# Kernel tuning notes

Hardware: AMD Instinct MI355X
Metric: run time of the kernel (lower is better)

## Reference

```python
import jax, jax.numpy as jnp
import numpy as np

SCALE = 1.0 / np.sqrt(64.0)  # module hardcodes 64**0.5, independent of d


def setup_inputs() -> dict:
    key = jax.random.key(0)
    k1, k2 = jax.random.split(key)
    x = jax.random.normal(k1, (8, 2048, 512), dtype=jnp.float32)
    kernel = jax.random.normal(k2, (3, 512, 512), dtype=jnp.float32) * 0.02
    return {"x": x, "kernel": kernel}


def reference(x, kernel):
    # x: [b, s, d]; kernel: [3, d, d]
    q = jnp.einsum('bsd,de->bse', x, kernel[0])
    k = jnp.einsum('bsd,de->bse', x, kernel[1])
    v = jnp.einsum('bsd,de->bse', x, kernel[2])
    scores = jnp.einsum('bqd,bkd->bqk', q, k) * SCALE  # [b, s, s]
    attn = jax.nn.softmax(scores, axis=-1)
    return jnp.einsum('bqk,bkd->bqd', attn, v)
```

## Files before the change

### kernel.cpp

```cpp
#include <hip/hip_runtime.h>


typedef unsigned short u16;
typedef unsigned int u32;

using bf16x8 = __attribute__((ext_vector_type(8))) short;
using f32x4  = __attribute__((ext_vector_type(4))) float;
using u16x4  = __attribute__((ext_vector_type(4))) u16;

__device__ __forceinline__ u16 f2bf(float f) {
  u32 u = __float_as_uint(f);
  u32 r = (u + 0x7FFFu + ((u >> 16) & 1u)) >> 16;
  return (u16)r;
}
__device__ __forceinline__ float bf2f(u16 h) {
  return __uint_as_float(((u32)h) << 16);
}

#define GLL16(src, dst)                                                        \
  __builtin_amdgcn_global_load_lds(                                            \
      (const __attribute__((address_space(1))) void*)(src),                    \
      (__attribute__((address_space(3))) void*)(dst), 16, 0, 0)

template <int K>
__device__ __forceinline__ void gemm8p_256x128(
    const u16* __restrict__ A0, const u16* __restrict__ B0,
    u16* lds, f32x4 (&acc)[4][4])
{
  const int tid = threadIdx.x;
  const int w = tid >> 6, l = tid & 63;
  const int wm = w >> 1, wn = w & 1;
  const int fr = l & 15;
  const int laneChunk = ((l >> 4) ^ ((fr >> 1) & 3)) << 3;
  const int laneA = (wm * 64 + fr) * 32 + laneChunk;
  const int laneB = (wn * 64 + fr) * 32 + laneChunk;
  u16* const ldsA = lds;
  u16* const ldsB = lds + 24576;

  const int chunkS = ((tid & 3) ^ ((tid >> 3) & 3)) << 3;
  const int r0 = tid >> 2;
  const u16* const sA0 = A0 + (size_t)r0 * K + chunkS;
  const u16* const sA1 = A0 + (size_t)(r0 + 128) * K + chunkS;
  const u16* const sB0 = B0 + (size_t)r0 * K + chunkS;
  const int dOf = w * 512;

#define PSTAGE_A(j, slot) do {                                                 \
    u16* d_ = ldsA + (slot) * 8192 + dOf;                                      \
    GLL16(sA0 + (j) * 32, d_);                                                 \
    GLL16(sA1 + (j) * 32, d_ + 4096);                                          \
  } while (0)
#define PSTAGE_B(j, slot) do {                                                 \
    u16* d_ = ldsB + (slot) * 4096 + dOf;                                      \
    GLL16(sB0 + (j) * 32, d_);                                                 \
  } while (0)

  PSTAGE_B(0, 0); PSTAGE_A(0, 0);
  PSTAGE_B(1, 1); PSTAGE_A(1, 1);

  constexpr int NS = K / 32;
  int slot = 0;
  for (int j = 0; j < NS; ++j) {
    const int jn = (j + 2 < NS) ? (j + 2) : (NS - 1);
    int slotn = slot + 2; if (slotn >= 3) slotn -= 3;

    asm volatile("s_waitcnt vmcnt(3)\n\ts_barrier" ::: "memory");

    const u16* const Ab = ldsA + slot * 8192;
    const u16* const Bb = ldsB + slot * 4096;
    bf16x8 a[4], b[4];
#pragma unroll
    for (int i = 0; i < 4; ++i) a[i] = *(const bf16x8*)(Ab + laneA + i * 512);
#pragma unroll
    for (int i = 0; i < 4; ++i) b[i] = *(const bf16x8*)(Bb + laneB + i * 512);
    PSTAGE_B(jn, slotn);
    __builtin_amdgcn_s_setprio(1);
#pragma unroll
    for (int mi = 0; mi < 2; ++mi)
#pragma unroll
      for (int nj = 0; nj < 4; ++nj)
        acc[mi][nj] = __builtin_amdgcn_mfma_f32_16x16x32_bf16(a[mi], b[nj], acc[mi][nj], 0, 0, 0);
    __builtin_amdgcn_s_setprio(0);
    PSTAGE_A(jn, slotn);
    __builtin_amdgcn_s_setprio(1);
#pragma unroll
    for (int mi = 2; mi < 4; ++mi)
#pragma unroll
      for (int nj = 0; nj < 4; ++nj)
        acc[mi][nj] = __builtin_amdgcn_mfma_f32_16x16x32_bf16(a[mi], b[nj], acc[mi][nj], 0, 0, 0);
    __builtin_amdgcn_s_setprio(0);

    slot = (slot == 2) ? 0 : slot + 1;
  }
#undef PSTAGE_A
#undef PSTAGE_B
}


__global__ void convert_x_kernel(const float* __restrict__ x, u16* __restrict__ xb) {
  int i = blockIdx.x * 256 + threadIdx.x;
  float4 f = ((const float4*)x)[i];
  u16x4 o = { f2bf(f.x), f2bf(f.y), f2bf(f.z), f2bf(f.w) };
  ((u16x4*)xb)[i] = o;
}

__global__ void convw_kernel(const float* __restrict__ W, u16* __restrict__ wT) {
  __shared__ float tile[32][33];
  const int mtx = blockIdx.z;
  const int e0 = blockIdx.x * 32, d0 = blockIdx.y * 32;
  const int tx = threadIdx.x, ty = threadIdx.y;
  const float* Wm = W + (size_t)mtx * 262144;
#pragma unroll
  for (int i = 0; i < 32; i += 8)
    tile[ty + i][tx] = Wm[(size_t)(d0 + ty + i) * 512 + e0 + tx];
  __syncthreads();
  u16* T = wT + (size_t)mtx * 262144;
#pragma unroll
  for (int i = 0; i < 32; i += 8)
    T[(size_t)(e0 + ty + i) * 512 + d0 + tx] = f2bf(tile[tx][ty + i]);
}

__global__ __launch_bounds__(512, 4) void gemm_qkv128_kernel(
    const u16* __restrict__ xb, const u16* __restrict__ wT,
    u16* __restrict__ qb, u16* __restrict__ kb, u16* __restrict__ vt)
{
  __shared__ __align__(16) u16 lds[36864];
  const int id = blockIdx.x;
  const int xcd = id & 7, t = id >> 3;
  const int n0 = (t % 12) * 128;
  const int m0 = (xcd * 8 + t / 12) * 256;
  f32x4 acc[4][4] = {};
  gemm8p_256x128<512>(xb + (size_t)m0 * 512, wT + (size_t)n0 * 512, lds, acc);

  const int tid = threadIdx.x, w = tid >> 6, l = tid & 63;
  const int wm = w >> 1, wn = w & 1;
  const int which = n0 >> 9;
  const int eb = (n0 & 511) + wn * 64 + (l & 15);
  const int rb = m0 + wm * 64 + (l >> 4) * 4;
  if (which < 2) {
    u16* dst = which ? kb : qb;
#pragma unroll
    for (int mi = 0; mi < 4; ++mi)
#pragma unroll
      for (int nj = 0; nj < 4; ++nj) {
        const int row = rb + mi * 16;
        const int col = eb + nj * 16;
#pragma unroll
        for (int r = 0; r < 4; ++r)
          dst[(size_t)(row + r) * 512 + col] = f2bf(acc[mi][nj][r]);
      }
  } else {
#pragma unroll
    for (int mi = 0; mi < 4; ++mi)
#pragma unroll
      for (int nj = 0; nj < 4; ++nj) {
        const int s = rb + mi * 16;
        const int b = s >> 11, sl = s & 2047;
        const int e = eb + nj * 16;
        u16x4 pk;
#pragma unroll
        for (int r = 0; r < 4; ++r) pk[r] = f2bf(acc[mi][nj][r]);
        *(u16x4*)(vt + (size_t)b * 1048576 + (size_t)e * 2048 + sl) = pk;
      }
  }
}

__global__ __launch_bounds__(512, 4) void gemm_scores128_kernel(
    const u16* __restrict__ qb, const u16* __restrict__ kb, u16* __restrict__ attn)
{
  __shared__ __align__(16) u16 lds[36864];
  const int id = blockIdx.x;
  const int z = id & 7, t = id >> 3;
  const int n0 = (t & 15) * 128;
  const int m0 = (t >> 4) * 256;
  f32x4 acc[4][4] = {};
  gemm8p_256x128<512>(qb + (size_t)z * 1048576 + (size_t)m0 * 512,
                      kb + (size_t)z * 1048576 + (size_t)n0 * 512, lds, acc);

  const int tid = threadIdx.x, w = tid >> 6, l = tid & 63;
  const int wm = w >> 1, wn = w & 1;
  u16* C = attn + (size_t)z * 4194304;
  const int rb = m0 + wm * 64 + (l >> 4) * 4;
  const int cb = n0 + wn * 64 + (l & 15);
#pragma unroll
  for (int mi = 0; mi < 4; ++mi)
#pragma unroll
    for (int nj = 0; nj < 4; ++nj) {
      const int row = rb + mi * 16;
      const int col = cb + nj * 16;
#pragma unroll
      for (int r = 0; r < 4; ++r)
        C[(size_t)(row + r) * 2048 + col] = f2bf(acc[mi][nj][r] * 0.125f);
    }
}

__global__ __launch_bounds__(256) void softmax_kernel(u16* __restrict__ attn) {
  __shared__ float reds[4];
  const size_t row = blockIdx.x;
  u16* p = attn + row * 2048;
  const int t = threadIdx.x, w = t >> 6, l = t & 63;

  uint4 u = ((const uint4*)p)[t];
  u16* us = (u16*)&u;
  float e[8], s = 0.f;
#pragma unroll
  for (int i = 0; i < 8; ++i) { e[i] = __expf(bf2f(us[i])); s += e[i]; }
  for (int off = 32; off >= 1; off >>= 1) s += __shfl_xor(s, off);
  if (l == 0) reds[w] = s;
  __syncthreads();
  s = reds[0] + reds[1] + reds[2] + reds[3];
  const float inv = 1.f / s;

#pragma unroll
  for (int i = 0; i < 8; ++i) us[i] = f2bf(e[i] * inv);
  ((uint4*)p)[t] = u;
}

__global__ __launch_bounds__(512, 2) void gemm_pv8p_kernel(
    const u16* __restrict__ attn, const u16* __restrict__ vt, float* __restrict__ out)
{
  __shared__ __align__(16) u16 lds[36864];
  const int id = blockIdx.x;
  const int z = id & 7;
  const int j = id >> 3;
  const int n0 = (j & 3) * 128;
  const int m0 = (j >> 2) * 256;
  f32x4 acc[4][4] = {};
  gemm8p_256x128<2048>(attn + (size_t)z * 4194304 + (size_t)m0 * 2048,
                       vt + (size_t)z * 1048576 + (size_t)n0 * 2048, lds, acc);

  const int tid = threadIdx.x, w = tid >> 6, l = tid & 63;
  const int wm = w >> 1, wn = w & 1;
  float* C = out + (size_t)z * 1048576;
  const int rb = m0 + wm * 64 + (l >> 4) * 4;
  const int cb = n0 + wn * 64 + (l & 15);
#pragma unroll
  for (int mi = 0; mi < 4; ++mi)
#pragma unroll
    for (int nj = 0; nj < 4; ++nj) {
      const int row = rb + mi * 16;
      const int col = cb + nj * 16;
#pragma unroll
      for (int r = 0; r < 4; ++r)
        C[(size_t)(row + r) * 512 + col] = acc[mi][nj][r];
    }
}

extern "C" void kernel_launch(void* const* d_in, const int* in_sizes, int n_in,
                              void* d_out, int out_size, void* d_ws, size_t ws_size,
                              hipStream_t stream) {
  const float* x = (const float*)d_in[0];
  const float* W = (const float*)d_in[1];
  float* out = (float*)d_out;

  if (ws_size < 117440512) return;
  u16* wsu  = (u16*)d_ws;
  u16* qb   = wsu;
  u16* kb   = qb + 8388608;
  u16* vt   = kb + 8388608;
  u16* attn = vt + 8388608;
  u16* xb   = attn;
  u16* wT   = attn + 8388608;

  convert_x_kernel<<<8192, 256, 0, stream>>>(x, xb);
  convw_kernel<<<dim3(16, 16, 3), dim3(32, 8), 0, stream>>>(W, wT);
  gemm_qkv128_kernel<<<768, 512, 0, stream>>>(xb, wT, qb, kb, vt);
  gemm_scores128_kernel<<<1024, 512, 0, stream>>>(qb, kb, attn);
  softmax_kernel<<<16384, 256, 0, stream>>>(attn);
  gemm_pv8p_kernel<<<256, 512, 0, stream>>>(attn, vt, out);
}
```

Baseline: 145.3 us.

## Double-buffer MFMA fragments in registers and deepen global prefetch to three stages

Restructures the shared GEMM main loop so each iteration issues the global-to-LDS loads for stage j+3 and reads the next stage's A/B fragments into a second register set, while MFMAs run on fragments already in registers. The loop is unrolled by two to ping-pong between the two register sets, and the barrier now waits on both vmcnt and lgkmcnt. The aim is to hide LDS read latency behind the MFMAs and keep more global loads in flight. Launch bounds drop from 4 to 2 blocks per CU on the QKV and scores GEMMs, which gives the compiler room for the extra fragment registers but may reduce occupancy.

```diff
diff --git a/kernel.cpp b/kernel.cpp
--- a/kernel.cpp
+++ b/kernel.cpp
@@ -53,44 +53,50 @@
     u16* d_ = ldsB + (slot) * 4096 + dOf;                                      \
     GLL16(sB0 + (j) * 32, d_);                                                 \
   } while (0)
+#define RDFRAG(sR, AV, BV) do {                                                \
+    const u16* Ab_ = ldsA + (sR) * 8192;                                       \
+    const u16* Bb_ = ldsB + (sR) * 4096;                                       \
+    _Pragma("unroll")                                                          \
+    for (int i_ = 0; i_ < 4; ++i_)                                             \
+      AV[i_] = *(const bf16x8*)(Ab_ + laneA + i_ * 512);                       \
+    _Pragma("unroll")                                                          \
+    for (int i_ = 0; i_ < 4; ++i_)                                             \
+      BV[i_] = *(const bf16x8*)(Bb_ + laneB + i_ * 512);                       \
+  } while (0)
+
+  constexpr int NS = K / 32;
+  bf16x8 aP[4], bP[4], aQ[4], bQ[4];
 
   PSTAGE_B(0, 0); PSTAGE_A(0, 0);
   PSTAGE_B(1, 1); PSTAGE_A(1, 1);
-
-  constexpr int NS = K / 32;
-  int slot = 0;
-  for (int j = 0; j < NS; ++j) {
-    const int jn = (j + 2 < NS) ? (j + 2) : (NS - 1);
-    int slotn = slot + 2; if (slotn >= 3) slotn -= 3;
-
-    asm volatile("s_waitcnt vmcnt(3)\n\ts_barrier" ::: "memory");
-
-    const u16* const Ab = ldsA + slot * 8192;
-    const u16* const Bb = ldsB + slot * 4096;
-    bf16x8 a[4], b[4];
-#pragma unroll
-    for (int i = 0; i < 4; ++i) a[i] = *(const bf16x8*)(Ab + laneA + i * 512);
-#pragma unroll
-    for (int i = 0; i < 4; ++i) b[i] = *(const bf16x8*)(Bb + laneB + i * 512);
-    PSTAGE_B(jn, slotn);
-    __builtin_amdgcn_s_setprio(1);
-#pragma unroll
-    for (int mi = 0; mi < 2; ++mi)
-#pragma unroll
-      for (int nj = 0; nj < 4; ++nj)
-        acc[mi][nj] = __builtin_amdgcn_mfma_f32_16x16x32_bf16(a[mi], b[nj], acc[mi][nj], 0, 0, 0);
-    __builtin_amdgcn_s_setprio(0);
-    PSTAGE_A(jn, slotn);
-    __builtin_amdgcn_s_setprio(1);
-#pragma unroll
-    for (int mi = 2; mi < 4; ++mi)
-#pragma unroll
-      for (int nj = 0; nj < 4; ++nj)
-        acc[mi][nj] = __builtin_amdgcn_mfma_f32_16x16x32_bf16(a[mi], b[nj], acc[mi][nj], 0, 0, 0);
-    __builtin_amdgcn_s_setprio(0);
-
-    slot = (slot == 2) ? 0 : slot + 1;
+  PSTAGE_B(2, 2); PSTAGE_A(2, 2);
+  asm volatile("s_waitcnt vmcnt(6)\n\ts_barrier" ::: "memory");
+  RDFRAG(0, aP, bP);
+
+#define GITER(jj, CA, CB, NA, NB) do {                                         \
+    const int js_ = ((jj) + 3 < NS) ? (jj) + 3 : NS - 1;                       \
+    const int sS_ = (jj) % 3;                                                  \
+    const int sR_ = ((jj) + 1) % 3;                                            \
+    asm volatile("s_waitcnt vmcnt(3) lgkmcnt(0)\n\ts_barrier" ::: "memory");   \
+    PSTAGE_B(js_, sS_);                                                        \
+    PSTAGE_A(js_, sS_);                                                        \
+    RDFRAG(sR_, NA, NB);                                                       \
+    __builtin_amdgcn_s_setprio(1);                                             \
+    _Pragma("unroll")                                                          \
+    for (int mi = 0; mi < 4; ++mi)                                             \
+      _Pragma("unroll")                                                        \
+      for (int nj = 0; nj < 4; ++nj)                                           \
+        acc[mi][nj] = __builtin_amdgcn_mfma_f32_16x16x32_bf16(                 \
+            CA[mi], CB[nj], acc[mi][nj], 0, 0, 0);                             \
+    __builtin_amdgcn_s_setprio(0);                                             \
+  } while (0)
+
+  for (int j = 0; j < NS; j += 2) {
+    GITER(j, aP, bP, aQ, bQ);
+    GITER(j + 1, aQ, bQ, aP, bP);
   }
+#undef GITER
+#undef RDFRAG
 #undef PSTAGE_A
 #undef PSTAGE_B
 }
@@ -119,7 +125,7 @@
     T[(size_t)(e0 + ty + i) * 512 + d0 + tx] = f2bf(tile[tx][ty + i]);
 }
 
-__global__ __launch_bounds__(512, 4) void gemm_qkv128_kernel(
+__global__ __launch_bounds__(512, 2) void gemm_qkv128_kernel(
     const u16* __restrict__ xb, const u16* __restrict__ wT,
     u16* __restrict__ qb, u16* __restrict__ kb, u16* __restrict__ vt)
 {
@@ -164,7 +170,7 @@
   }
 }
 
-__global__ __launch_bounds__(512, 4) void gemm_scores128_kernel(
+__global__ __launch_bounds__(512, 2) void gemm_scores128_kernel(
     const u16* __restrict__ qb, const u16* __restrict__ kb, u16* __restrict__ attn)
 {
   __shared__ __align__(16) u16 lds[36864];
```

Result: slower. 152.7 us (+5.1%).

## Use 256x256 tiles for the QK^T scores GEMM

Applied to the files above, without the earlier changes.

Adds a new 256x256 tile GEMM routine in which each wave computes a 128x64 sub-tile, and uses it for the scores kernel, halving the grid to 512 blocks. Larger tiles raise arithmetic intensity and cut the global reloads of Q and K. The cost is double the accumulator registers, more LDS and lower occupancy (launch bounds 2), and with only 512 blocks the tail may be less balanced. The launch bounds hint on the PV kernel also changes from 2 to 4.

```diff
diff --git a/kernel.cpp b/kernel.cpp
--- a/kernel.cpp
+++ b/kernel.cpp
@@ -95,6 +95,83 @@
 #undef PSTAGE_B
 }
 
+template <int K>
+__device__ __forceinline__ void gemm8p_256sq(
+    const u16* __restrict__ A0, const u16* __restrict__ B0,
+    u16* lds, f32x4 (&acc)[8][4])
+{
+  const int tid = threadIdx.x;
+  const int w = tid >> 6, l = tid & 63;
+  const int wm = w >> 2, wn = w & 3;
+  const int fr = l & 15;
+  const int laneChunk = ((l >> 4) ^ ((fr >> 1) & 3)) << 3;
+  const int laneA = (wm * 128 + fr) * 32 + laneChunk;
+  const int laneB = (wn * 64 + fr) * 32 + laneChunk;
+  u16* const ldsA = lds;
+  u16* const ldsB = lds + 24576;
+
+  const int chunkS = ((tid & 3) ^ ((tid >> 3) & 3)) << 3;
+  const int r0 = tid >> 2;
+  const u16* const sA0 = A0 + (size_t)r0 * K + chunkS;
+  const u16* const sA1 = A0 + (size_t)(r0 + 128) * K + chunkS;
+  const u16* const sB0 = B0 + (size_t)r0 * K + chunkS;
+  const u16* const sB1 = B0 + (size_t)(r0 + 128) * K + chunkS;
+  const int dOf = w * 512;
+
+#define SSTAGE_A(j, slot) do {                                                 \
+    u16* d_ = ldsA + (slot) * 8192 + dOf;                                      \
+    GLL16(sA0 + (j) * 32, d_);                                                 \
+    GLL16(sA1 + (j) * 32, d_ + 4096);                                          \
+  } while (0)
+#define SSTAGE_B(j, slot) do {                                                 \
+    u16* d_ = ldsB + (slot) * 8192 + dOf;                                      \
+    GLL16(sB0 + (j) * 32, d_);                                                 \
+    GLL16(sB1 + (j) * 32, d_ + 4096);                                          \
+  } while (0)
+
+  SSTAGE_B(0, 0); SSTAGE_A(0, 0);
+  SSTAGE_B(1, 1); SSTAGE_A(1, 1);
+
+  constexpr int NS = K / 32;
+  int slot = 0;
+  for (int j = 0; j < NS; ++j) {
+    const int jn = (j + 2 < NS) ? (j + 2) : (NS - 1);
+    int slotn = slot + 2; if (slotn >= 3) slotn -= 3;
+
+    asm volatile("s_waitcnt vmcnt(4)\n\ts_barrier" ::: "memory");
+
+    const u16* const Ab = ldsA + slot * 8192;
+    const u16* const Bb = ldsB + slot * 8192;
+    bf16x8 b[4], a0[4], a1[4];
+#pragma unroll
+    for (int i = 0; i < 4; ++i) b[i]  = *(const bf16x8*)(Bb + laneB + i * 512);
+#pragma unroll
+    for (int i = 0; i < 4; ++i) a0[i] = *(const bf16x8*)(Ab + laneA + i * 512);
+    SSTAGE_A(jn, slotn);
+    __builtin_amdgcn_s_setprio(1);
+#pragma unroll
+    for (int mi = 0; mi < 4; ++mi)
+#pragma unroll
+      for (int nj = 0; nj < 4; ++nj)
+        acc[mi][nj] = __builtin_amdgcn_mfma_f32_16x16x32_bf16(a0[mi], b[nj], acc[mi][nj], 0, 0, 0);
+    __builtin_amdgcn_s_setprio(0);
+#pragma unroll
+    for (int i = 0; i < 4; ++i) a1[i] = *(const bf16x8*)(Ab + laneA + (4 + i) * 512);
+    SSTAGE_B(jn, slotn);
+    __builtin_amdgcn_s_setprio(1);
+#pragma unroll
+    for (int mi = 0; mi < 4; ++mi)
+#pragma unroll
+      for (int nj = 0; nj < 4; ++nj)
+        acc[4 + mi][nj] = __builtin_amdgcn_mfma_f32_16x16x32_bf16(a1[mi], b[nj], acc[4 + mi][nj], 0, 0, 0);
+    __builtin_amdgcn_s_setprio(0);
+
+    slot = (slot == 2) ? 0 : slot + 1;
+  }
+#undef SSTAGE_A
+#undef SSTAGE_B
+}
+
 
 __global__ void convert_x_kernel(const float* __restrict__ x, u16* __restrict__ xb) {
   int i = blockIdx.x * 256 + threadIdx.x;
@@ -164,25 +241,25 @@
   }
 }
 
-__global__ __launch_bounds__(512, 4) void gemm_scores128_kernel(
+__global__ __launch_bounds__(512, 2) void gemm_scores256_kernel(
     const u16* __restrict__ qb, const u16* __restrict__ kb, u16* __restrict__ attn)
 {
-  __shared__ __align__(16) u16 lds[36864];
+  __shared__ __align__(16) u16 lds[49152];
   const int id = blockIdx.x;
   const int z = id & 7, t = id >> 3;
-  const int n0 = (t & 15) * 128;
-  const int m0 = (t >> 4) * 256;
-  f32x4 acc[4][4] = {};
-  gemm8p_256x128<512>(qb + (size_t)z * 1048576 + (size_t)m0 * 512,
-                      kb + (size_t)z * 1048576 + (size_t)n0 * 512, lds, acc);
+  const int n0 = (t & 7) * 256;
+  const int m0 = (t >> 3) * 256;
+  f32x4 acc[8][4] = {};
+  gemm8p_256sq<512>(qb + (size_t)z * 1048576 + (size_t)m0 * 512,
+                    kb + (size_t)z * 1048576 + (size_t)n0 * 512, lds, acc);
 
   const int tid = threadIdx.x, w = tid >> 6, l = tid & 63;
-  const int wm = w >> 1, wn = w & 1;
+  const int wm = w >> 2, wn = w & 3;
   u16* C = attn + (size_t)z * 4194304;
-  const int rb = m0 + wm * 64 + (l >> 4) * 4;
+  const int rb = m0 + wm * 128 + (l >> 4) * 4;
   const int cb = n0 + wn * 64 + (l & 15);
 #pragma unroll
-  for (int mi = 0; mi < 4; ++mi)
+  for (int mi = 0; mi < 8; ++mi)
 #pragma unroll
     for (int nj = 0; nj < 4; ++nj) {
       const int row = rb + mi * 16;
@@ -215,7 +292,7 @@
   ((uint4*)p)[t] = u;
 }
 
-__global__ __launch_bounds__(512, 2) void gemm_pv8p_kernel(
+__global__ __launch_bounds__(512, 4) void gemm_pv8p_kernel(
     const u16* __restrict__ attn, const u16* __restrict__ vt, float* __restrict__ out)
 {
   __shared__ __align__(16) u16 lds[36864];
@@ -264,7 +341,7 @@
   convert_x_kernel<<<8192, 256, 0, stream>>>(x, xb);
   convw_kernel<<<dim3(16, 16, 3), dim3(32, 8), 0, stream>>>(W, wT);
   gemm_qkv128_kernel<<<768, 512, 0, stream>>>(xb, wT, qb, kb, vt);
-  gemm_scores128_kernel<<<1024, 512, 0, stream>>>(qb, kb, attn);
+  gemm_scores256_kernel<<<512, 512, 0, stream>>>(qb, kb, attn);
   softmax_kernel<<<16384, 256, 0, stream>>>(attn);
   gemm_pv8p_kernel<<<256, 512, 0, stream>>>(attn, vt, out);
 }
```

After: 143.4 us. Within noise of the previous version (-1.3%).
